# Kernel tuning notes

Hardware: AMD Instinct MI355X
Metric: run time of the kernel (lower is better)

Reference implementation:

```python
import jax, jax.numpy as jnp
import numpy as np

MARGIN = 1.0
GAMMA = 0.99
N = 16384
N_POS = 2048
DATA_LEN = 100000

def setup_inputs() -> dict:
    key = jax.random.key(0)
    k1, k2, k3 = jax.random.split(key, 3)
    y_pred = jax.random.normal(k1, (N,), dtype=jnp.float32)
    # positives occupy the first N_POS slots so the boolean gather is a static slice
    y_true = jnp.concatenate([jnp.ones((N_POS,), jnp.float32), jnp.zeros((N - N_POS,), jnp.float32)])
    u_all = jax.random.uniform(k2, (DATA_LEN,), dtype=jnp.float32)
    u_pos = jax.random.uniform(k3, (DATA_LEN,), dtype=jnp.float32)
    index_s = jnp.arange(N, dtype=jnp.int32)  # unique sample indices into u buffers
    return {"y_pred": y_pred, "y_true": y_true, "u_all": u_all, "u_pos": u_pos, "index_s": index_s, "n_pos": N_POS}

def reference(y_pred, y_true, u_all, u_pos, index_s, n_pos):
    # positives are the first n_pos entries by construction (see setup_inputs)
    f_ps = y_pred[:n_pos]                      # (P,)
    index_ps = index_s[:n_pos]                 # (P,)
    pos_mask = (y_true == 1.0).astype(y_pred.dtype)  # (n,)
    # pairwise squared hinge: (P, n)
    diff = MARGIN - (f_ps[:, None] - y_pred[None, :])
    sur_loss = jnp.maximum(diff, 0.0) ** 2
    pos_sur_loss = sur_loss * pos_mask[None, :]
    # moving-average state update at the positive sample indices (gather + scatter)
    u_all_new = (1.0 - GAMMA) * u_all[index_ps] + GAMMA * sur_loss.mean(axis=1)    # (P,)
    u_pos_new = (1.0 - GAMMA) * u_pos[index_ps] + GAMMA * pos_sur_loss.mean(axis=1)  # (P,)
    # p is detached in the original (p.detach_())
    p = (u_pos_new[:, None] - u_all_new[:, None] * pos_mask[None, :]) / (u_all_new[:, None] ** 2)  # (P, n)
    p = jax.lax.stop_gradient(p)
    loss = jnp.mean(p * sur_loss)
    return loss
```

## Files before the change

kernel.cpp:

```cpp
#include <hip/hip_runtime.h>


constexpr int BLOCK = 256;

__global__ __launch_bounds__(BLOCK) void aploss_rows(
    const float* __restrict__ y_pred,
    const float* __restrict__ y_true,
    const float* __restrict__ u_all,
    const float* __restrict__ u_pos,
    const int*   __restrict__ index_s,
    double*      __restrict__ row_out,
    int n)
{
    const int i   = blockIdx.x;
    const int tid = threadIdx.x;
    const float f_i = y_pred[i];

    const float4* yp4 = (const float4*)y_pred;
    const float4* yt4 = (const float4*)y_true;
    const int n4 = n >> 2;

    double s_all = 0.0, s_pos = 0.0;
    for (int j = tid; j < n4; j += BLOCK) {
        float4 yp = yp4[j];
        float4 yt = yt4[j];
        float sa = 0.f, sp = 0.f;
        float d, s;
        d = 1.0f - (f_i - yp.x); d = fmaxf(d, 0.f); s = d * d; sa += s; sp += (yt.x == 1.0f) ? s : 0.f;
        d = 1.0f - (f_i - yp.y); d = fmaxf(d, 0.f); s = d * d; sa += s; sp += (yt.y == 1.0f) ? s : 0.f;
        d = 1.0f - (f_i - yp.z); d = fmaxf(d, 0.f); s = d * d; sa += s; sp += (yt.z == 1.0f) ? s : 0.f;
        d = 1.0f - (f_i - yp.w); d = fmaxf(d, 0.f); s = d * d; sa += s; sp += (yt.w == 1.0f) ? s : 0.f;
        s_all += (double)sa;
        s_pos += (double)sp;
    }

    #pragma unroll
    for (int off = 32; off > 0; off >>= 1) {
        s_all += __shfl_down(s_all, off, 64);
        s_pos += __shfl_down(s_pos, off, 64);
    }

    __shared__ double sh_all[BLOCK / 64];
    __shared__ double sh_pos[BLOCK / 64];
    const int wave = tid >> 6;
    const int lane = tid & 63;
    if (lane == 0) { sh_all[wave] = s_all; sh_pos[wave] = s_pos; }
    __syncthreads();

    if (tid == 0) {
        double ta = sh_all[0] + sh_all[1] + sh_all[2] + sh_all[3];
        double tp = sh_pos[0] + sh_pos[1] + sh_pos[2] + sh_pos[3];
        const int idx = index_s[i];
        const double inv_n = 1.0 / (double)n;
        const double ua = 0.01 * (double)u_all[idx] + 0.99 * (ta * inv_n);
        const double up = 0.01 * (double)u_pos[idx] + 0.99 * (tp * inv_n);
        row_out[i] = (up * ta - ua * tp) / (ua * ua);
    }
}

__global__ __launch_bounds__(BLOCK) void aploss_reduce(
    const double* __restrict__ row_terms,
    float* __restrict__ out,
    int n_pos, int n)
{
    const int tid = threadIdx.x;
    double s = 0.0;
    for (int i = tid; i < n_pos; i += BLOCK) s += row_terms[i];
    #pragma unroll
    for (int off = 32; off > 0; off >>= 1) s += __shfl_down(s, off, 64);

    __shared__ double sh[BLOCK / 64];
    const int wave = tid >> 6;
    const int lane = tid & 63;
    if (lane == 0) sh[wave] = s;
    __syncthreads();
    if (tid == 0) {
        double tot = sh[0] + sh[1] + sh[2] + sh[3];
        out[0] = (float)(tot / ((double)n_pos * (double)n));
    }
}

extern "C" void kernel_launch(void* const* d_in, const int* in_sizes, int n_in,
                              void* d_out, int out_size, void* d_ws, size_t ws_size,
                              hipStream_t stream) {
    const float* y_pred  = (const float*)d_in[0];
    const float* y_true  = (const float*)d_in[1];
    const float* u_all   = (const float*)d_in[2];
    const float* u_pos   = (const float*)d_in[3];
    const int*   index_s = (const int*)d_in[4];
    const int n     = in_sizes[0];
    const int n_pos = 2048;

    double* row_terms = (double*)d_ws;
    float*  out       = (float*)d_out;

    aploss_rows<<<n_pos, BLOCK, 0, stream>>>(y_pred, y_true, u_all, u_pos,
                                             index_s, row_terms, n);
    aploss_reduce<<<1, BLOCK, 0, stream>>>(row_terms, out, n_pos, n);
}
```

Measured before the change: 75.93 us.

## Process eight positive rows per block to reuse loaded prediction tiles

Each block now handles 8 positive rows with 512 threads, so every float4 of y_pred/y_true loaded from memory is reused across 8 rows instead of one. Per-thread accumulation moves from double to float with FMA, and the positive mask becomes a multiply by y_true instead of a compare. Cutting global/L2 traffic and the costly double-precision adds should reduce the time, but float accumulation can lose accuracy, the grid shrinks to 256 blocks, and multiplying by y_true only matches the mask because the labels are exactly 0 or 1.

Result: faster. 71.90 us (-5.3%).

```diff
diff --git a/kernel.cpp b/kernel.cpp
--- a/kernel.cpp
+++ b/kernel.cpp
@@ -1,9 +1,10 @@
 #include <hip/hip_runtime.h>
 
 
-constexpr int BLOCK = 256;
+constexpr int ROWS    = 8;
+constexpr int THREADS = 512;
 
-__global__ __launch_bounds__(BLOCK) void aploss_rows(
+__global__ __launch_bounds__(THREADS) void aploss_rows(
     const float* __restrict__ y_pred,
     const float* __restrict__ y_true,
     const float* __restrict__ u_all,
@@ -12,64 +13,82 @@
     double*      __restrict__ row_out,
     int n)
 {
-    const int i   = blockIdx.x;
+    const int i0  = blockIdx.x * ROWS;
     const int tid = threadIdx.x;
-    const float f_i = y_pred[i];
+
+    float f[ROWS];
+    #pragma unroll
+    for (int r = 0; r < ROWS; ++r) f[r] = y_pred[i0 + r];
 
     const float4* yp4 = (const float4*)y_pred;
     const float4* yt4 = (const float4*)y_true;
     const int n4 = n >> 2;
 
-    double s_all = 0.0, s_pos = 0.0;
-    for (int j = tid; j < n4; j += BLOCK) {
-        float4 yp = yp4[j];
-        float4 yt = yt4[j];
-        float sa = 0.f, sp = 0.f;
-        float d, s;
-        d = 1.0f - (f_i - yp.x); d = fmaxf(d, 0.f); s = d * d; sa += s; sp += (yt.x == 1.0f) ? s : 0.f;
-        d = 1.0f - (f_i - yp.y); d = fmaxf(d, 0.f); s = d * d; sa += s; sp += (yt.y == 1.0f) ? s : 0.f;
-        d = 1.0f - (f_i - yp.z); d = fmaxf(d, 0.f); s = d * d; sa += s; sp += (yt.z == 1.0f) ? s : 0.f;
-        d = 1.0f - (f_i - yp.w); d = fmaxf(d, 0.f); s = d * d; sa += s; sp += (yt.w == 1.0f) ? s : 0.f;
-        s_all += (double)sa;
-        s_pos += (double)sp;
+    float sa[ROWS], sp[ROWS];
+    #pragma unroll
+    for (int r = 0; r < ROWS; ++r) { sa[r] = 0.f; sp[r] = 0.f; }
+
+    for (int j = tid; j < n4; j += THREADS) {
+        const float4 yp = yp4[j];
+        const float4 yt = yt4[j];
+        const float c0 = 1.0f + yp.x, c1 = 1.0f + yp.y;
+        const float c2 = 1.0f + yp.z, c3 = 1.0f + yp.w;
+        #pragma unroll
+        for (int r = 0; r < ROWS; ++r) {
+            float m, t;
+            m = fmaxf(c0 - f[r], 0.f); sa[r] = fmaf(m, m, sa[r]); t = m * yt.x; sp[r] = fmaf(t, m, sp[r]);
+            m = fmaxf(c1 - f[r], 0.f); sa[r] = fmaf(m, m, sa[r]); t = m * yt.y; sp[r] = fmaf(t, m, sp[r]);
+            m = fmaxf(c2 - f[r], 0.f); sa[r] = fmaf(m, m, sa[r]); t = m * yt.z; sp[r] = fmaf(t, m, sp[r]);
+            m = fmaxf(c3 - f[r], 0.f); sa[r] = fmaf(m, m, sa[r]); t = m * yt.w; sp[r] = fmaf(t, m, sp[r]);
+        }
     }
 
     #pragma unroll
     for (int off = 32; off > 0; off >>= 1) {
-        s_all += __shfl_down(s_all, off, 64);
-        s_pos += __shfl_down(s_pos, off, 64);
+        #pragma unroll
+        for (int r = 0; r < ROWS; ++r) {
+            sa[r] += __shfl_down(sa[r], off, 64);
+            sp[r] += __shfl_down(sp[r], off, 64);
+        }
     }
 
-    __shared__ double sh_all[BLOCK / 64];
-    __shared__ double sh_pos[BLOCK / 64];
+    __shared__ float sh_a[THREADS / 64][ROWS];
+    __shared__ float sh_p[THREADS / 64][ROWS];
     const int wave = tid >> 6;
     const int lane = tid & 63;
-    if (lane == 0) { sh_all[wave] = s_all; sh_pos[wave] = s_pos; }
+    if (lane == 0) {
+        #pragma unroll
+        for (int r = 0; r < ROWS; ++r) { sh_a[wave][r] = sa[r]; sh_p[wave][r] = sp[r]; }
+    }
     __syncthreads();
 
-    if (tid == 0) {
-        double ta = sh_all[0] + sh_all[1] + sh_all[2] + sh_all[3];
-        double tp = sh_pos[0] + sh_pos[1] + sh_pos[2] + sh_pos[3];
-        const int idx = index_s[i];
+    if (tid < ROWS) {
+        double ta = 0.0, tp = 0.0;
+        #pragma unroll
+        for (int w = 0; w < THREADS / 64; ++w) {
+            ta += (double)sh_a[w][tid];
+            tp += (double)sh_p[w][tid];
+        }
+        const int idx = index_s[i0 + tid];
         const double inv_n = 1.0 / (double)n;
         const double ua = 0.01 * (double)u_all[idx] + 0.99 * (ta * inv_n);
         const double up = 0.01 * (double)u_pos[idx] + 0.99 * (tp * inv_n);
-        row_out[i] = (up * ta - ua * tp) / (ua * ua);
+        row_out[i0 + tid] = (up * ta - ua * tp) / (ua * ua);
     }
 }
 
-__global__ __launch_bounds__(BLOCK) void aploss_reduce(
+__global__ __launch_bounds__(256) void aploss_reduce(
     const double* __restrict__ row_terms,
     float* __restrict__ out,
     int n_pos, int n)
 {
     const int tid = threadIdx.x;
     double s = 0.0;
-    for (int i = tid; i < n_pos; i += BLOCK) s += row_terms[i];
+    for (int i = tid; i < n_pos; i += 256) s += row_terms[i];
     #pragma unroll
     for (int off = 32; off > 0; off >>= 1) s += __shfl_down(s, off, 64);
 
-    __shared__ double sh[BLOCK / 64];
+    __shared__ double sh[4];
     const int wave = tid >> 6;
     const int lane = tid & 63;
     if (lane == 0) sh[wave] = s;
@@ -94,7 +113,7 @@
     double* row_terms = (double*)d_ws;
     float*  out       = (float*)d_out;
 
-    aploss_rows<<<n_pos, BLOCK, 0, stream>>>(y_pred, y_true, u_all, u_pos,
-                                             index_s, row_terms, n);
-    aploss_reduce<<<1, BLOCK, 0, stream>>>(row_terms, out, n_pos, n);
+    aploss_rows<<<n_pos / ROWS, THREADS, 0, stream>>>(
+        y_pred, y_true, u_all, u_pos, index_s, row_terms, n);
+    aploss_reduce<<<1, 256, 0, stream>>>(row_terms, out, n_pos, n);
 }
```
